# Performance work log

Hardware: AMD Instinct MI355X
Metric: run time of the kernel (lower is better)

Reference implementation:

```python
import jax, jax.numpy as jnp
import numpy as np

MARGIN = 0.1
LAMBDA_EFFECT = 0.5

B, T_V, K, T_S = 32, 8192, 64, 128


def setup_inputs() -> dict:
    key = jax.random.key(0)
    k1, k2, k3, k4, k5 = jax.random.split(key, 5)
    pred_orig = jax.random.normal(k1, (B, T_V), dtype=jnp.float32)
    pred_intervened = jax.random.normal(k2, (K, B, T_V), dtype=jnp.float32)
    intervened_indices = jax.random.randint(k3, (K,), 0, T_S, dtype=jnp.int32)
    # GT alignment mask: sparse-ish binary alignment between frames and sentences
    gt_mask = jax.random.bernoulli(k4, 0.2, (B, T_V, T_S)).astype(jnp.int32)
    # prefix-valid video mask: valid length per batch in [T_V//2, T_V]
    lengths = jax.random.randint(k5, (B,), T_V // 2, T_V + 1, dtype=jnp.int32)
    mask_video = (jnp.arange(T_V, dtype=jnp.int32)[None, :] < lengths[:, None]).astype(jnp.int32)
    return {
        "pred_orig": pred_orig,
        "pred_intervened": pred_intervened,
        "intervened_indices": intervened_indices,
        "gt_mask": gt_mask,
        "mask_video": mask_video,
    }


def reference(pred_orig, pred_intervened, intervened_indices, gt_mask, mask_video):
    # pred_orig: [B,T], pred_intervened: [K,B,T], gt_mask: [B,T,S], mask_video: [B,T]
    prob_orig = jax.nn.sigmoid(pred_orig)                 # [B,T]
    prob_int = jax.nn.sigmoid(pred_intervened)            # [K,B,T]
    effect = jnp.abs(prob_orig[None, :, :] - prob_int)    # [K,B,T]

    valid = mask_video.astype(bool)                       # [B,T] (prefix mask == :T_v_valid slice)
    # gather intervened sentence columns: [B,T,K] -> [K,B,T]
    gt_sel = jnp.transpose(gt_mask[:, :, intervened_indices], (2, 0, 1))

    aligned = (gt_sel > 0) & valid[None]                  # [K,B,T]
    non_aligned = (gt_sel == 0) & valid[None]             # [K,B,T]

    cnt_a = aligned.sum(axis=-1)                          # [K,B]
    cnt_n = non_aligned.sum(axis=-1)                      # [K,B]

    ea = jnp.sum(effect * aligned, axis=-1) / jnp.maximum(cnt_a, 1)
    en = jnp.sum(effect * non_aligned, axis=-1) / jnp.maximum(cnt_n, 1)

    per_pair = jnp.where((cnt_a > 0) & (cnt_n > 0),
                         jax.nn.relu(MARGIN - (ea - en)),
                         jnp.zeros_like(ea))
    num_interventions = pred_orig.shape[0] * pred_intervened.shape[0]
    alignment_consistency = per_pair.sum() / max(num_interventions, 1)
    total_intervention_loss = alignment_consistency * LAMBDA_EFFECT
    return alignment_consistency, total_intervention_loss
```

## Files before the change

### kernel.cpp

```cpp
#include <hip/hip_runtime.h>
#include <cstdint>

#define BB 32
#define TV 8192
#define KK 64
#define TS 128
#define MARGIN_F 0.1f
#define LAMBDA_F 0.5f

#define TT 256
static constexpr int KSTR = BB * TV;
static constexpr int NTILE = TV / TT;


__global__ __launch_bounds__(256, 4) void fused_kernel(
    const float* __restrict__ po, const float* __restrict__ pi,
    const int* __restrict__ idx, const int* __restrict__ gt,
    const int* __restrict__ mv,
    float* __restrict__ gsa, float* __restrict__ gsv,
    float* __restrict__ gca, int* __restrict__ len) {
  const int tid = threadIdx.x;
  const int lane = tid & 63;
  const int w = tid >> 6;
  const int tile = blockIdx.x & (NTILE - 1);
  const int b = blockIdx.x >> 5;
  const int t0 = tile * TT;

  __shared__ unsigned long long planes[4][65];
  __shared__ unsigned long long sVg[4];
  __shared__ float so[TT];
  __shared__ float saL[KK][65];
  __shared__ float svL[KK][65];

  const int r0 = b * TV + t0 + w * 64;
  const unsigned long long V = __ballot(mv[r0 + lane] != 0);
  if (lane == 0) {
    sVg[w] = V;
    if (V) atomicAdd(&len[b], __popcll(V));
  }
  so[tid] = __fdividef(1.f, 1.f + __expf(-po[b * TV + t0 + tid]));

  const int c = idx[lane];
  const int csel = c & 3, csh = c >> 2;
  unsigned long long plane = 0ull;
  if (V != 0ull) {
    const int4* rowp = (const int4*)(gt + (size_t)r0 * TS);
#pragma unroll 4
    for (int ch = 0; ch < 32; ++ch) {
      int4 v = rowp[ch * 64 + lane];
      unsigned long long b0 = __ballot(v.x > 0);
      unsigned long long b1 = __ballot(v.y > 0);
      unsigned long long b2 = __ballot(v.z > 0);
      unsigned long long b3 = __ballot(v.w > 0);
      unsigned long long sel =
          (csel == 0) ? b0 : (csel == 1) ? b1 : (csel == 2) ? b2 : b3;
      const unsigned long long raw0 = (sel >> csh) & 1ull;
      const unsigned long long raw1 = (sel >> (32 + csh)) & 1ull;
      plane |= (raw0 << (2 * ch)) | (raw1 << (2 * ch + 1));
    }
    plane &= V;
  }
  planes[w][lane] = plane;
  __syncthreads();

  if ((sVg[0] | sVg[1] | sVg[2] | sVg[3]) == 0ull) return;

  const int g = lane >> 4;
  const int sh4 = (lane & 15) * 4;
  const unsigned vb4 = (unsigned)((sVg[g] >> sh4) & 15ull);
  const float4 so4 = *(const float4*)&so[lane * 4];
  const float* pib = pi + (size_t)b * TV + t0 + lane * 4;

#pragma unroll 4
  for (int kk = 0; kk < 16; ++kk) {
    const int k = w * 16 + kk;
    const float4 xi = *(const float4*)(pib + (size_t)k * KSTR);
    const unsigned ab4 = (unsigned)((planes[g][k] >> sh4) & 15ull);
    float sa = 0.f, sv = 0.f;
    {
      const float e = fabsf(so4.x - __fdividef(1.f, 1.f + __expf(-xi.x)));
      if (ab4 & 1u) sa += e;
      if (vb4 & 1u) sv += e;
    }
    {
      const float e = fabsf(so4.y - __fdividef(1.f, 1.f + __expf(-xi.y)));
      if (ab4 & 2u) sa += e;
      if (vb4 & 2u) sv += e;
    }
    {
      const float e = fabsf(so4.z - __fdividef(1.f, 1.f + __expf(-xi.z)));
      if (ab4 & 4u) sa += e;
      if (vb4 & 4u) sv += e;
    }
    {
      const float e = fabsf(so4.w - __fdividef(1.f, 1.f + __expf(-xi.w)));
      if (ab4 & 8u) sa += e;
      if (vb4 & 8u) sv += e;
    }
    saL[k][lane] = sa;
    svL[k][lane] = sv;
  }
  __syncthreads();

  if (tid < KK) {
    const int k = tid;
    float S = 0.f;
    int ca = 0;
#pragma unroll 8
    for (int j = 0; j < 64; ++j) S += saL[k][j];
#pragma unroll
    for (int gg = 0; gg < 4; ++gg) ca += __popcll(planes[gg][k]);
    atomicAdd(&gsa[k * BB + b], S);
    if (ca) atomicAdd(&gca[k * BB + b], (float)ca);
  } else if (tid < 2 * KK) {
    const int k = tid - KK;
    float S = 0.f;
#pragma unroll 8
    for (int j = 0; j < 64; ++j) S += svL[k][j];
    atomicAdd(&gsv[k * BB + b], S);
  }
}

__global__ __launch_bounds__(256) void fin_kernel(
    const float* __restrict__ gsa, const float* __restrict__ gsv,
    const float* __restrict__ gca, const int* __restrict__ len,
    float* __restrict__ out) {
  float s = 0.f;
  for (int i = threadIdx.x; i < KK * BB; i += 256) {
    const int b = i & (BB - 1);
    const float ca = gca[i];
    const float cn = (float)len[b] - ca;
    if (ca > 0.f && cn > 0.f) {
      const float sa = gsa[i];
      const float sv = gsv[i];
      const float d = MARGIN_F - (sa / ca - (sv - sa) / cn);
      s += d > 0.f ? d : 0.f;
    }
  }
#pragma unroll
  for (int off = 32; off > 0; off >>= 1) s += __shfl_down(s, off);
  __shared__ float ws4[4];
  if ((threadIdx.x & 63) == 0) ws4[threadIdx.x >> 6] = s;
  __syncthreads();
  if (threadIdx.x == 0) {
    const float S = ws4[0] + ws4[1] + ws4[2] + ws4[3];
    const float ac = S * (1.0f / (float)(KK * BB));
    out[0] = ac;
    out[1] = ac * LAMBDA_F;
  }
}

extern "C" void kernel_launch(void* const* d_in, const int* in_sizes, int n_in,
                              void* d_out, int out_size, void* d_ws, size_t ws_size,
                              hipStream_t stream) {
  const float* pred_orig = (const float*)d_in[0];
  const float* pred_int  = (const float*)d_in[1];
  const int*   idx       = (const int*)d_in[2];
  const int*   gt        = (const int*)d_in[3];
  const int*   mv        = (const int*)d_in[4];
  float* out = (float*)d_out;

  float* gsa = (float*)d_ws;
  float* gsv = gsa + KK * BB;
  float* gca = gsv + KK * BB;
  int*   len = (int*)(gca + KK * BB);

  hipMemsetAsync(d_ws, 0, (size_t)(3 * KK * BB) * sizeof(float) + BB * sizeof(int),
                 stream);
  fused_kernel<<<BB * NTILE, 256, 0, stream>>>(
      pred_orig, pred_int, idx, gt, mv, gsa, gsv, gca, len);
  fin_kernel<<<1, 256, 0, stream>>>(gsa, gsv, gca, len, out);
}
```

Measured before the change: 263.8 us.

## Software-pipeline gt loads and reduce partial sums with wave shuffles

The gt mask loop now prefetches the next four int4 chunks while ballots run on the current four, so more memory requests are in flight. The pred_intervened loop issues four float4 loads before computing. Per-k partial sums are folded across lanes with shuffles down to 8 values, which shrinks the shared-memory staging arrays and the final serial sum. This adds register pressure that could reduce occupancy under the launch bound of 4 blocks per SM.

```diff
diff --git a/kernel.cpp b/kernel.cpp
--- a/kernel.cpp
+++ b/kernel.cpp
@@ -29,8 +29,8 @@
   __shared__ unsigned long long planes[4][65];
   __shared__ unsigned long long sVg[4];
   __shared__ float so[TT];
-  __shared__ float saL[KK][65];
-  __shared__ float svL[KK][65];
+  __shared__ float saL[KK][9];
+  __shared__ float svL[KK][9];
 
   const int r0 = b * TV + t0 + w * 64;
   const unsigned long long V = __ballot(mv[r0 + lane] != 0);
@@ -43,11 +43,11 @@
   const int c = idx[lane];
   const int csel = c & 3, csh = c >> 2;
   unsigned long long plane = 0ull;
+
   if (V != 0ull) {
-    const int4* rowp = (const int4*)(gt + (size_t)r0 * TS);
-#pragma unroll 4
-    for (int ch = 0; ch < 32; ++ch) {
-      int4 v = rowp[ch * 64 + lane];
+    const int4* rowp = (const int4*)(gt + (size_t)r0 * TS) + lane;
+
+    auto procA = [&](int4 v, int ch) {
       unsigned long long b0 = __ballot(v.x > 0);
       unsigned long long b1 = __ballot(v.y > 0);
       unsigned long long b2 = __ballot(v.z > 0);
@@ -57,6 +57,23 @@
       const unsigned long long raw0 = (sel >> csh) & 1ull;
       const unsigned long long raw1 = (sel >> (32 + csh)) & 1ull;
       plane |= (raw0 << (2 * ch)) | (raw1 << (2 * ch + 1));
+    };
+
+    int4 v0 = rowp[0 * 64], v1 = rowp[1 * 64], v2 = rowp[2 * 64], v3 = rowp[3 * 64];
+#pragma unroll
+    for (int ch = 0; ch < 32; ch += 4) {
+      int4 n0 = v0, n1 = v1, n2 = v2, n3 = v3;
+      if (ch + 4 < 32) {
+        n0 = rowp[(ch + 4) * 64];
+        n1 = rowp[(ch + 5) * 64];
+        n2 = rowp[(ch + 6) * 64];
+        n3 = rowp[(ch + 7) * 64];
+      }
+      procA(v0, ch);
+      procA(v1, ch + 1);
+      procA(v2, ch + 2);
+      procA(v3, ch + 3);
+      v0 = n0; v1 = n1; v2 = n2; v3 = n3;
     }
     plane &= V;
   }
@@ -71,10 +88,7 @@
   const float4 so4 = *(const float4*)&so[lane * 4];
   const float* pib = pi + (size_t)b * TV + t0 + lane * 4;
 
-#pragma unroll 4
-  for (int kk = 0; kk < 16; ++kk) {
-    const int k = w * 16 + kk;
-    const float4 xi = *(const float4*)(pib + (size_t)k * KSTR);
+  auto procB = [&](float4 xi, int k) {
     const unsigned ab4 = (unsigned)((planes[g][k] >> sh4) & 15ull);
     float sa = 0.f, sv = 0.f;
     {
@@ -97,27 +111,40 @@
       if (ab4 & 8u) sa += e;
       if (vb4 & 8u) sv += e;
     }
-    saL[k][lane] = sa;
-    svL[k][lane] = sv;
+    sa += __shfl_down(sa, 32);
+    sv += __shfl_down(sv, 32);
+    sa += __shfl_down(sa, 16);
+    sv += __shfl_down(sv, 16);
+    sa += __shfl_down(sa, 8);
+    sv += __shfl_down(sv, 8);
+    if (lane < 8) { saL[k][lane] = sa; svL[k][lane] = sv; }
+  };
+
+#pragma unroll
+  for (int kk = 0; kk < 16; kk += 4) {
+    const int k0 = w * 16 + kk;
+    const float4 x0 = *(const float4*)(pib + (size_t)(k0 + 0) * KSTR);
+    const float4 x1 = *(const float4*)(pib + (size_t)(k0 + 1) * KSTR);
+    const float4 x2 = *(const float4*)(pib + (size_t)(k0 + 2) * KSTR);
+    const float4 x3 = *(const float4*)(pib + (size_t)(k0 + 3) * KSTR);
+    procB(x0, k0 + 0);
+    procB(x1, k0 + 1);
+    procB(x2, k0 + 2);
+    procB(x3, k0 + 3);
   }
   __syncthreads();
 
   if (tid < KK) {
     const int k = tid;
-    float S = 0.f;
+    float SA = 0.f, SV = 0.f;
+#pragma unroll
+    for (int j = 0; j < 8; ++j) { SA += saL[k][j]; SV += svL[k][j]; }
     int ca = 0;
-#pragma unroll 8
-    for (int j = 0; j < 64; ++j) S += saL[k][j];
 #pragma unroll
     for (int gg = 0; gg < 4; ++gg) ca += __popcll(planes[gg][k]);
-    atomicAdd(&gsa[k * BB + b], S);
+    atomicAdd(&gsa[k * BB + b], SA);
+    atomicAdd(&gsv[k * BB + b], SV);
     if (ca) atomicAdd(&gca[k * BB + b], (float)ca);
-  } else if (tid < 2 * KK) {
-    const int k = tid - KK;
-    float S = 0.f;
-#pragma unroll 8
-    for (int j = 0; j < 64; ++j) S += svL[k][j];
-    atomicAdd(&gsv[k * BB + b], S);
   }
 }
 
```

Result: no change. 264.7 us (+0.3%).

## Process two time tiles per block with software-pipelined gt and pred loads

Applied to the files above, without the earlier changes.

Each block now handles two tiles (tile i and i+16) of the same batch. The gt-mask bit extraction for the second tile is interleaved with the effect computation for the first tile, and loads are issued in explicit register batches to keep more memory requests in flight. Per-k partial sums are held in registers across both tiles and reduced once, which halves the shared-memory reductions and atomics per tile. Launch bounds drop to 2 blocks/SM and register pressure rises, which could reduce occupancy.

```diff
diff --git a/kernel.cpp b/kernel.cpp
--- a/kernel.cpp
+++ b/kernel.cpp
@@ -13,7 +13,11 @@
 static constexpr int NTILE = TV / TT;
 
 
-__global__ __launch_bounds__(256, 4) void fused_kernel(
+__device__ __forceinline__ float sigf(float x) {
+  return __fdividef(1.f, 1.f + __expf(-x));
+}
+
+__global__ __launch_bounds__(256, 2) void fused_kernel(
     const float* __restrict__ po, const float* __restrict__ pi,
     const int* __restrict__ idx, const int* __restrict__ gt,
     const int* __restrict__ mv,
@@ -22,102 +26,194 @@
   const int tid = threadIdx.x;
   const int lane = tid & 63;
   const int w = tid >> 6;
-  const int tile = blockIdx.x & (NTILE - 1);
-  const int b = blockIdx.x >> 5;
-  const int t0 = tile * TT;
-
-  __shared__ unsigned long long planes[4][65];
-  __shared__ unsigned long long sVg[4];
-  __shared__ float so[TT];
+  const int b = blockIdx.x >> 4;
+  const int ti0 = blockIdx.x & 15;
+  const int t0[2] = {ti0 * TT, (ti0 + 16) * TT};
+
+  __shared__ unsigned long long planes[2][4][65];
+  __shared__ unsigned long long sVg[2][4];
+  __shared__ float so_s[2][TT];
   __shared__ float saL[KK][65];
   __shared__ float svL[KK][65];
 
-  const int r0 = b * TV + t0 + w * 64;
-  const unsigned long long V = __ballot(mv[r0 + lane] != 0);
-  if (lane == 0) {
-    sVg[w] = V;
-    if (V) atomicAdd(&len[b], __popcll(V));
-  }
-  so[tid] = __fdividef(1.f, 1.f + __expf(-po[b * TV + t0 + tid]));
-
   const int c = idx[lane];
   const int csel = c & 3, csh = c >> 2;
-  unsigned long long plane = 0ull;
-  if (V != 0ull) {
-    const int4* rowp = (const int4*)(gt + (size_t)r0 * TS);
-#pragma unroll 4
-    for (int ch = 0; ch < 32; ++ch) {
-      int4 v = rowp[ch * 64 + lane];
-      unsigned long long b0 = __ballot(v.x > 0);
-      unsigned long long b1 = __ballot(v.y > 0);
-      unsigned long long b2 = __ballot(v.z > 0);
-      unsigned long long b3 = __ballot(v.w > 0);
-      unsigned long long sel =
-          (csel == 0) ? b0 : (csel == 1) ? b1 : (csel == 2) ? b2 : b3;
-      const unsigned long long raw0 = (sel >> csh) & 1ull;
-      const unsigned long long raw1 = (sel >> (32 + csh)) & 1ull;
-      plane |= (raw0 << (2 * ch)) | (raw1 << (2 * ch + 1));
-    }
-    plane &= V;
-  }
-  planes[w][lane] = plane;
-  __syncthreads();
-
-  if ((sVg[0] | sVg[1] | sVg[2] | sVg[3]) == 0ull) return;
+
+  unsigned long long Vw[2];
+#pragma unroll
+  for (int i = 0; i < 2; ++i) {
+    const int rr = b * TV + t0[i] + w * 64;
+    Vw[i] = __ballot(mv[rr + lane] != 0);
+    if (lane == 0) {
+      sVg[i][w] = Vw[i];
+      if (Vw[i]) atomicAdd(&len[b], (int)__popcll(Vw[i]));
+    }
+    so_s[i][tid] = sigf(po[b * TV + t0[i] + tid]);
+  }
+  __syncthreads();
+  const bool t1v = (sVg[1][0] | sVg[1][1] | sVg[1][2] | sVg[1][3]) != 0ull;
 
   const int g = lane >> 4;
   const int sh4 = (lane & 15) * 4;
-  const unsigned vb4 = (unsigned)((sVg[g] >> sh4) & 15ull);
-  const float4 so4 = *(const float4*)&so[lane * 4];
-  const float* pib = pi + (size_t)b * TV + t0 + lane * 4;
-
-#pragma unroll 4
+  float4 so4[2];
+  unsigned vb4[2];
+#pragma unroll
+  for (int i = 0; i < 2; ++i) {
+    so4[i] = *(const float4*)&so_s[i][lane * 4];
+    vb4[i] = (unsigned)((sVg[i][g] >> sh4) & 15ull);
+  }
+
+  auto procA = [&](int4 v, int r2, unsigned long long& pl) {
+    unsigned long long b0 = __ballot(v.x > 0);
+    unsigned long long b1 = __ballot(v.y > 0);
+    unsigned long long b2 = __ballot(v.z > 0);
+    unsigned long long b3 = __ballot(v.w > 0);
+    unsigned long long sel =
+        (csel == 0) ? b0 : (csel == 1) ? b1 : (csel == 2) ? b2 : b3;
+    pl |= ((sel >> csh) & 1ull) << r2;
+    pl |= ((sel >> (32 + csh)) & 1ull) << (r2 + 1);
+  };
+
+  const int4* g0p = (const int4*)(gt + (size_t)(b * TV + t0[0] + w * 64) * TS) + lane;
+  unsigned long long plane0 = 0ull;
+  {
+    int4 X[8], Y[8];
+#pragma unroll
+    for (int q = 0; q < 8; ++q) X[q] = g0p[q * 64];
+#pragma unroll
+    for (int q = 0; q < 8; ++q) Y[q] = g0p[(8 + q) * 64];
+#pragma unroll
+    for (int q = 0; q < 8; ++q) procA(X[q], 0 * 16 + 2 * q, plane0);
+#pragma unroll
+    for (int q = 0; q < 8; ++q) X[q] = g0p[(16 + q) * 64];
+#pragma unroll
+    for (int q = 0; q < 8; ++q) procA(Y[q], 1 * 16 + 2 * q, plane0);
+#pragma unroll
+    for (int q = 0; q < 8; ++q) Y[q] = g0p[(24 + q) * 64];
+#pragma unroll
+    for (int q = 0; q < 8; ++q) procA(X[q], 2 * 16 + 2 * q, plane0);
+#pragma unroll
+    for (int q = 0; q < 8; ++q) procA(Y[q], 3 * 16 + 2 * q, plane0);
+  }
+  plane0 &= Vw[0];
+  planes[0][w][lane] = plane0;
+  __syncthreads();
+
+  float sa[16], sv[16];
+#pragma unroll
+  for (int q = 0; q < 16; ++q) { sa[q] = 0.f; sv[q] = 0.f; }
+
+  const float* pib[2] = {pi + (size_t)b * TV + t0[0] + lane * 4,
+                         pi + (size_t)b * TV + t0[1] + lane * 4};
+
+  auto issueP = [&](float4 (&Q)[4], int grp, int i) {
+#pragma unroll
+    for (int q = 0; q < 4; ++q)
+      Q[q] = *(const float4*)(pib[i] + (size_t)(16 * w + grp * 4 + q) * KSTR);
+  };
+  auto procBgrp = [&](float4 (&Q)[4], int grp, int i) {
+#pragma unroll
+    for (int q = 0; q < 4; ++q) {
+      const int kk = grp * 4 + q;
+      const int k = 16 * w + kk;
+      const unsigned ab4 = (unsigned)((planes[i][g][k] >> sh4) & 15ull);
+      const float4 xi = Q[q];
+      float e;
+      e = fabsf(so4[i].x - sigf(xi.x));
+      if (ab4 & 1u) sa[kk] += e;
+      if (vb4[i] & 1u) sv[kk] += e;
+      e = fabsf(so4[i].y - sigf(xi.y));
+      if (ab4 & 2u) sa[kk] += e;
+      if (vb4[i] & 2u) sv[kk] += e;
+      e = fabsf(so4[i].z - sigf(xi.z));
+      if (ab4 & 4u) sa[kk] += e;
+      if (vb4[i] & 4u) sv[kk] += e;
+      e = fabsf(so4[i].w - sigf(xi.w));
+      if (ab4 & 8u) sa[kk] += e;
+      if (vb4[i] & 8u) sv[kk] += e;
+    }
+  };
+
+  const int4* g1p = (const int4*)(gt + (size_t)(b * TV + t0[1] + w * 64) * TS) + lane;
+  unsigned long long plane1 = 0ull;
+  {
+    float4 q0[4], q1[4];
+    int4 P0[8], P1[8];
+    issueP(q0, 0, 0);
+    if (t1v) {
+#pragma unroll
+      for (int q = 0; q < 8; ++q) P0[q] = g1p[q * 64];
+    }
+    issueP(q1, 1, 0);
+    if (t1v) {
+#pragma unroll
+      for (int q = 0; q < 8; ++q) P1[q] = g1p[(8 + q) * 64];
+    }
+    procBgrp(q0, 0, 0);
+    if (t1v) {
+#pragma unroll
+      for (int q = 0; q < 8; ++q) procA(P0[q], 0 * 16 + 2 * q, plane1);
+    }
+    issueP(q0, 2, 0);
+    if (t1v) {
+#pragma unroll
+      for (int q = 0; q < 8; ++q) P0[q] = g1p[(16 + q) * 64];
+    }
+    procBgrp(q1, 1, 0);
+    if (t1v) {
+#pragma unroll
+      for (int q = 0; q < 8; ++q) procA(P1[q], 1 * 16 + 2 * q, plane1);
+    }
+    issueP(q1, 3, 0);
+    if (t1v) {
+#pragma unroll
+      for (int q = 0; q < 8; ++q) P1[q] = g1p[(24 + q) * 64];
+    }
+    procBgrp(q0, 2, 0);
+    if (t1v) {
+#pragma unroll
+      for (int q = 0; q < 8; ++q) procA(P0[q], 2 * 16 + 2 * q, plane1);
+    }
+    procBgrp(q1, 3, 0);
+    if (t1v) {
+#pragma unroll
+      for (int q = 0; q < 8; ++q) procA(P1[q], 3 * 16 + 2 * q, plane1);
+    }
+  }
+  plane1 &= Vw[1];
+  planes[1][w][lane] = t1v ? plane1 : 0ull;
+  __syncthreads();
+
+  if (t1v) {
+    float4 q0[4], q1[4];
+    issueP(q0, 0, 1);
+    issueP(q1, 1, 1);
+    procBgrp(q0, 0, 1);
+    issueP(q0, 2, 1);
+    procBgrp(q1, 1, 1);
+    issueP(q1, 3, 1);
+    procBgrp(q0, 2, 1);
+    procBgrp(q1, 3, 1);
+  }
+
+#pragma unroll
   for (int kk = 0; kk < 16; ++kk) {
-    const int k = w * 16 + kk;
-    const float4 xi = *(const float4*)(pib + (size_t)k * KSTR);
-    const unsigned ab4 = (unsigned)((planes[g][k] >> sh4) & 15ull);
-    float sa = 0.f, sv = 0.f;
-    {
-      const float e = fabsf(so4.x - __fdividef(1.f, 1.f + __expf(-xi.x)));
-      if (ab4 & 1u) sa += e;
-      if (vb4 & 1u) sv += e;
-    }
-    {
-      const float e = fabsf(so4.y - __fdividef(1.f, 1.f + __expf(-xi.y)));
-      if (ab4 & 2u) sa += e;
-      if (vb4 & 2u) sv += e;
-    }
-    {
-      const float e = fabsf(so4.z - __fdividef(1.f, 1.f + __expf(-xi.z)));
-      if (ab4 & 4u) sa += e;
-      if (vb4 & 4u) sv += e;
-    }
-    {
-      const float e = fabsf(so4.w - __fdividef(1.f, 1.f + __expf(-xi.w)));
-      if (ab4 & 8u) sa += e;
-      if (vb4 & 8u) sv += e;
-    }
-    saL[k][lane] = sa;
-    svL[k][lane] = sv;
-  }
-  __syncthreads();
-
+    saL[16 * w + kk][lane] = sa[kk];
+    svL[16 * w + kk][lane] = sv[kk];
+  }
+  __syncthreads();
   if (tid < KK) {
     const int k = tid;
-    float S = 0.f;
+    float SA = 0.f, SV = 0.f;
+#pragma unroll 8
+    for (int j = 0; j < 64; ++j) { SA += saL[k][j]; SV += svL[k][j]; }
     int ca = 0;
-#pragma unroll 8
-    for (int j = 0; j < 64; ++j) S += saL[k][j];
-#pragma unroll
-    for (int gg = 0; gg < 4; ++gg) ca += __popcll(planes[gg][k]);
-    atomicAdd(&gsa[k * BB + b], S);
+#pragma unroll
+    for (int gg = 0; gg < 4; ++gg)
+      ca += __popcll(planes[0][gg][k]) + __popcll(planes[1][gg][k]);
+    atomicAdd(&gsa[k * BB + b], SA);
+    atomicAdd(&gsv[k * BB + b], SV);
     if (ca) atomicAdd(&gca[k * BB + b], (float)ca);
-  } else if (tid < 2 * KK) {
-    const int k = tid - KK;
-    float S = 0.f;
-#pragma unroll 8
-    for (int j = 0; j < 64; ++j) S += svL[k][j];
-    atomicAdd(&gsv[k * BB + b], S);
   }
 }
 
@@ -167,7 +263,7 @@
 
   hipMemsetAsync(d_ws, 0, (size_t)(3 * KK * BB) * sizeof(float) + BB * sizeof(int),
                  stream);
-  fused_kernel<<<BB * NTILE, 256, 0, stream>>>(
+  fused_kernel<<<BB * NTILE / 2, 256, 0, stream>>>(
       pred_orig, pred_int, idx, gt, mv, gsa, gsv, gca, len);
   fin_kernel<<<1, 256, 0, stream>>>(gsa, gsv, gca, len, out);
 }
```

After: 269.8 us. +2.3%, slower.
